# Performance work log

Measured on AMD Instinct MI355X. Metric: run time of the kernel, lower is better.

The kernel has to match this reference:

```python
import jax, jax.numpy as jnp
import numpy as np

LOG2 = float(np.log(2.0))

def _ssp(x):
    # shifted softplus: ln(0.5*(exp(x)+1)) = softplus(x) - ln 2
    return jax.nn.softplus(x) - LOG2

def setup_inputs() -> dict:
    key = jax.random.key(0)
    ks = jax.random.split(key, 8)
    B, N, D = 32, 512, 1024
    H = D // 2
    s = lambda fan_in: 1.0 / np.sqrt(fan_in)
    return {
        "representation": jax.random.normal(ks[0], (B, N, D), jnp.float32),
        "R": jax.random.normal(ks[1], (B, N, 3), jnp.float32),
        "atom_mask": jnp.ones((B, N), jnp.float32),
        "W1": jax.random.normal(ks[2], (D, H), jnp.float32) * s(D),
        "b1": jnp.zeros((H,), jnp.float32),
        "W2": jax.random.normal(ks[3], (H, 1), jnp.float32) * s(H),
        "b2": jnp.zeros((1,), jnp.float32),
        "Wc1": jax.random.normal(ks[4], (D, H), jnp.float32) * s(D),
        "bc1": jnp.zeros((H,), jnp.float32),
        "Wc2": jax.random.normal(ks[5], (H, 1), jnp.float32) * s(H),
        "bc2": jnp.zeros((1,), jnp.float32),
    }

def reference(representation, R, atom_mask, W1, b1, W2, b2, Wc1, bc1, Wc2, bc2):
    B, N, _ = representation.shape
    # Atomwise pyramidal MLP: n_in -> n_in//2 (shifted softplus) -> 1
    yi = _ssp(jnp.einsum("bnd,dh->bnh", representation, W1) + b1)
    yi = jnp.einsum("bnh,ho->bno", yi, W2) + b2            # [B,N,1]
    # masked sum pool over atoms (mean=0, stddev=1 so standardize is identity)
    y = jnp.sum(yi * atom_mask[..., None], axis=1)          # [B,1]

    # pairwise distances with safe sqrt (diag is exactly zero)
    diff = R[:, None, :, :] - R[:, :, None, :]              # [B,N,N,3]
    d2 = jnp.sum(diff * diff, axis=-1)                      # [B,N,N]
    dist = jnp.where(d2 > 0, jnp.sqrt(jnp.where(d2 > 0, d2, 1.0)), 0.0)

    eye = jnp.eye(N, dtype=dist.dtype)
    tot_mask = atom_mask[:, None, :] * atom_mask[:, :, None] * (1.0 - eye)
    keep = (tot_mask != 0).astype(dist.dtype)               # [B,N,N]
    dist = dist * keep

    # charge net: Dense(n_in, n_in//2, ssp) -> Dense(n_in//2, 1)
    q = _ssp(jnp.einsum("bnd,dh->bnh", representation, Wc1) + bc1)
    q = jnp.einsum("bnh,ho->bno", q, Wc2) + bc2             # [B,N,1]

    inv2 = (1e-5 + dist) ** -2                              # [B,N,N]
    coulomb = q[:, :, 0][:, None, :] * inv2 * q             # [B,N,N] (q_j * inv * q_i)
    coulomb = coulomb * keep
    e = jnp.sum(coulomb, axis=(1, 2))                       # [B]

    return y + e[:, None]                                   # [B,1]
```

## Files before the change

kernel.cpp:

```cpp
#include <hip/hip_runtime.h>
#include <math.h>


typedef unsigned short u16;
typedef unsigned int u32;
typedef __bf16 bf16x8 __attribute__((ext_vector_type(8)));
typedef float f32x4 __attribute__((ext_vector_type(4)));

#define GK 1024
#define NT 16

#define GLOAD_LDS16(g, l) __builtin_amdgcn_global_load_lds( \
    (const __attribute__((address_space(1))) void*)(g),     \
    (__attribute__((address_space(3))) void*)(l), 16, 0, 0)

__device__ __forceinline__ u16 f2bf(float f) {
    u32 u = __float_as_uint(f);
    return (u16)((u + 0x7FFFu + ((u >> 16) & 1u)) >> 16);
}

__device__ __forceinline__ float ssp_f(float x) {
    return __logf(0.5f * (__expf(x) + 1.0f));
}

__device__ __forceinline__ float ssp_slow(float x) {
    return fmaxf(x, 0.0f) + log1pf(expf(-fabsf(x))) - 0.6931471805599453f;
}


__global__ __launch_bounds__(256) void prep(
    const float* __restrict__ rep, const float* __restrict__ W1,
    const float* __restrict__ Wc1, u16* __restrict__ Abf,
    u16* __restrict__ Btb, float* __restrict__ out)
{
    __shared__ float tile[32][33];
    const int blk = blockIdx.x;
    const int t = threadIdx.x;
    if (blk < 8192) {
        int i = (blk * 256 + t) * 8;
        float4 x = *(const float4*)(rep + i);
        float4 y = *(const float4*)(rep + i + 4);
        union { u16 h[8]; uint4 v; } o;
        o.h[0] = f2bf(x.x); o.h[1] = f2bf(x.y); o.h[2] = f2bf(x.z); o.h[3] = f2bf(x.w);
        o.h[4] = f2bf(y.x); o.h[5] = f2bf(y.y); o.h[6] = f2bf(y.z); o.h[7] = f2bf(y.w);
        *(uint4*)(Abf + i) = o.v;
        if (blk == 0 && t < 32) out[t] = 0.0f;
    } else {
        const int bb = blk - 8192;
        const int k0 = (bb & 31) * 32;
        const int n0 = (bb >> 5) * 32;
        const float* src = (n0 < 512) ? W1 : Wc1;
        const int ns0 = (n0 < 512) ? n0 : n0 - 512;
#pragma unroll
        for (int j = 0; j < 4; j++) {
            int idx = j * 256 + t;
            int kl = idx >> 5, nl = idx & 31;
            tile[kl][nl] = src[(size_t)(k0 + kl) * 512 + ns0 + nl];
        }
        __syncthreads();
#pragma unroll
        for (int j = 0; j < 4; j++) {
            int idx = j * 256 + t;
            int nl = idx >> 5, kl = idx & 31;
            Btb[(size_t)(n0 + nl) * 1024 + k0 + kl] = f2bf(tile[kl][nl]);
        }
    }
}


__global__ __launch_bounds__(512, 2) void gemm_mfma(
    const u16* __restrict__ A,
    const u16* __restrict__ Bt,
    const float* __restrict__ b1, const float* __restrict__ W2,
    const float* __restrict__ bc1, const float* __restrict__ Wc2,
    float* __restrict__ parts)
{
    __shared__ u16 smem[2][32768];

    const int blk = blockIdx.x;
    const int swz = ((blk & 7) << 5) | (blk >> 3);
    const int bm = swz >> 2;
    const int bn = swz & 3;
    const int tid = threadIdx.x;
    const int w = tid >> 6, lane = tid & 63;
    const int wm = w & 1, wn = w >> 1;
    const int lm = lane & 15, q = lane >> 4;

    f32x4 acc[8][4];
#pragma unroll
    for (int i = 0; i < 8; i++)
#pragma unroll
        for (int j = 0; j < 4; j++)
            acc[i][j] = (f32x4){0.0f, 0.0f, 0.0f, 0.0f};

    int goff[2][2];
#pragma unroll
    for (int h = 0; h < 2; h++)
#pragma unroll
        for (int p2 = 0; p2 < 2; p2++) {
            int ci = h * 1024 + (w * 2 + p2) * 64 + lane;
            int row = ci >> 3;
            int c = (ci & 7) ^ (row & 7);
            goff[h][p2] = row * GK + c * 8;
        }

    int arow[4], brow[2], aswz[2];
#pragma unroll
    for (int mi = 0; mi < 4; mi++) arow[mi] = (wm * 128 + mi * 16 + lm) * 64;
#pragma unroll
    for (int nj = 0; nj < 2; nj++) brow[nj] = (wn * 64 + nj * 16 + lm) * 64;
#pragma unroll
    for (int kk = 0; kk < 2; kk++) aswz[kk] = ((kk * 4 + q) ^ (lm & 7)) * 8;

    const u16* Ab = A + (size_t)bm * 256 * GK;
    const u16* Bb = Bt + (size_t)bn * 256 * GK;

#define STAGE_HT(G, RG, H) do {                                               \
    GLOAD_LDS16((G) + goff[H][0], &smem[nxt][(RG) + ((H) * 1024 + (w * 2 + 0) * 64) * 8]); \
    GLOAD_LDS16((G) + goff[H][1], &smem[nxt][(RG) + ((H) * 1024 + (w * 2 + 1) * 64) * 8]); \
} while (0)

#define READ_A(MH)                                                            \
    _Pragma("unroll") for (int mi = 0; mi < 4; mi++)                          \
    _Pragma("unroll") for (int kk = 0; kk < 2; kk++)                          \
        afr[mi][kk] = *(const bf16x8*)&smem[cur][arow[mi] + (MH) * 4096 + aswz[kk]];

#define READ_B(NH)                                                            \
    _Pragma("unroll") for (int nj = 0; nj < 2; nj++)                          \
    _Pragma("unroll") for (int kk = 0; kk < 2; kk++)                          \
        bfr2[nj][kk] = *(const bf16x8*)&smem[cur][16384 + brow[nj] + (NH) * 2048 + aswz[kk]];

#define MFMA_QUAD(MH, NH)                                                     \
    _Pragma("unroll") for (int kk = 0; kk < 2; kk++)                          \
    _Pragma("unroll") for (int mi = 0; mi < 4; mi++)                          \
    _Pragma("unroll") for (int nj = 0; nj < 2; nj++)                          \
        acc[(MH) * 4 + mi][(NH) * 2 + nj] = __builtin_amdgcn_mfma_f32_16x16x32_bf16( \
            afr[mi][kk], bfr2[nj][kk], acc[(MH) * 4 + mi][(NH) * 2 + nj], 0, 0, 0);

    {
        const int nxt = 0;
#pragma unroll
        for (int h = 0; h < 2; h++) {
            STAGE_HT(Ab, 0, h);
            STAGE_HT(Bb, 16384, h);
        }
    }
    asm volatile("s_waitcnt vmcnt(0)" ::: "memory");
    __builtin_amdgcn_s_barrier();

    bf16x8 afr[4][2], bfr2[2][2];

    for (int t = 0; t < NT; ++t) {
        const int cur = t & 1, nxt = cur ^ 1;
        const bool st = (t < NT - 1);
        const u16* gA = Ab + ((t + 1) & (NT - 1)) * 64;
        const u16* gB = Bb + ((t + 1) & (NT - 1)) * 64;

        if (st) { STAGE_HT(gA, 0, 0); STAGE_HT(gB, 16384, 0); }
        READ_A(0); READ_B(0);
        __builtin_amdgcn_s_barrier();
        __builtin_amdgcn_s_setprio(1);
        MFMA_QUAD(0, 0);
        __builtin_amdgcn_s_setprio(0);
        __builtin_amdgcn_s_barrier();

        if (st) { STAGE_HT(gA, 0, 1); STAGE_HT(gB, 16384, 1); }
        READ_B(1);
        __builtin_amdgcn_s_barrier();
        __builtin_amdgcn_s_setprio(1);
        MFMA_QUAD(0, 1);
        __builtin_amdgcn_s_setprio(0);
        __builtin_amdgcn_s_barrier();

        READ_A(1);
        __builtin_amdgcn_s_barrier();
        __builtin_amdgcn_s_setprio(1);
        MFMA_QUAD(1, 1);
        __builtin_amdgcn_s_setprio(0);
        __builtin_amdgcn_s_barrier();

        READ_B(0);
        __builtin_amdgcn_s_barrier();
        __builtin_amdgcn_s_setprio(1);
        MFMA_QUAD(1, 0);
        __builtin_amdgcn_s_setprio(0);
        if (st) asm volatile("s_waitcnt vmcnt(0)" ::: "memory");
        __builtin_amdgcn_s_barrier();
    }

#undef STAGE_HT
#undef READ_A
#undef READ_B
#undef MFMA_QUAD

    __syncthreads();
    float* red = (float*)&smem[0][0];
    const bool is_q = (bn >= 2);
    const float* bb2 = is_q ? bc1 : b1;
    const float* vv = is_q ? Wc2 : W2;
    float bias[4], v[4];
#pragma unroll
    for (int nfr = 0; nfr < 4; nfr++) {
        int c = (bn & 1) * 256 + wn * 64 + nfr * 16 + lm;
        bias[nfr] = bb2[c];
        v[nfr] = vv[c];
    }
#pragma unroll
    for (int mfr = 0; mfr < 8; mfr++) {
#pragma unroll
        for (int r = 0; r < 4; r++) {
            float s = 0.0f;
#pragma unroll
            for (int nfr = 0; nfr < 4; nfr++)
                s += v[nfr] * ssp_f(acc[mfr][nfr][r] + bias[nfr]);
            s += __shfl_xor(s, 1);
            s += __shfl_xor(s, 2);
            s += __shfl_xor(s, 4);
            s += __shfl_xor(s, 8);
            if (lm == 0) red[wn * 256 + wm * 128 + mfr * 16 + q * 4 + r] = s;
        }
    }
    __syncthreads();
    if (tid < 256) {
        float val = red[0 * 256 + tid] + red[1 * 256 + tid] +
                    red[2 * 256 + tid] + red[3 * 256 + tid];
        parts[(size_t)bn * 16384 + bm * 256 + tid] = val;
    }
}


__global__ __launch_bounds__(256) void coulomb_k(
    const float* __restrict__ R, const float* __restrict__ mask,
    const float* __restrict__ parts, const float* __restrict__ b2p,
    const float* __restrict__ bc2p, float* __restrict__ out)
{
    const int N = 512;
    const int b = blockIdx.y;
    const int chunk = blockIdx.x;
    __shared__ float Rx[512], Ry[512], Rz[512], QM[512];
    __shared__ float rbuf[4];
    const int tid = threadIdx.x;
    const float bc2 = bc2p[0];
    const float b2 = b2p[0];

    for (int j = tid; j < N; j += 256) {
        int idx = b * N + j;
        float m = mask[idx];
        const float* rp = R + (size_t)idx * 3;
        Rx[j] = rp[0];
        Ry[j] = rp[1];
        Rz[j] = rp[2];
        float qv = parts[2 * 16384 + idx] + parts[3 * 16384 + idx] + bc2;
        QM[j] = qv * m;
    }
    __syncthreads();

    const int i = chunk * 64 + (tid & 63);
    const int js = (tid >> 6) * 128;
    const float xi = Rx[i], yi = Ry[i], zi = Rz[i], qmi = QM[i];
    float e = 0.0f;
    for (int j = js; j < js + 128; j++) {
        float dx = xi - Rx[j];
        float dy = yi - Ry[j];
        float dz = zi - Rz[j];
        float d2 = dx * dx + dy * dy + dz * dz;
        float t = 1e-5f + sqrtf(d2);
        float term = qmi * QM[j] / (t * t);
        e += (j == i) ? 0.0f : term;
    }
    if (tid < 64) {
        int ii = b * N + chunk * 64 + tid;
        float yv = parts[0 * 16384 + ii] + parts[1 * 16384 + ii] + b2;
        e += yv * mask[ii];
    }
    for (int off = 32; off > 0; off >>= 1) e += __shfl_down(e, off, 64);
    if ((tid & 63) == 0) rbuf[tid >> 6] = e;
    __syncthreads();
    if (tid == 0) atomicAdd(&out[b], rbuf[0] + rbuf[1] + rbuf[2] + rbuf[3]);
}


#define BM 128
#define BN 64
#define BK 16

__global__ __launch_bounds__(256) void mlp_gemm(
    const float* __restrict__ A, const float* __restrict__ W1,
    const float* __restrict__ Wc1, const float* __restrict__ b1,
    const float* __restrict__ bc1, const float* __restrict__ W2,
    const float* __restrict__ Wc2, float* __restrict__ yi_part,
    float* __restrict__ q_part)
{
    const int K = 1024;
    const int bm = blockIdx.x;
    const int bn = blockIdx.y;
    const bool is_q = (bn >= 8);
    const float* __restrict__ W = is_q ? Wc1 : W1;
    const int j0 = (bn & 7) * BN;

    __shared__ float As[BK][BM + 4];
    __shared__ float Bs[BK][BN + 4];
    __shared__ float red[BM];

    const int tid = threadIdx.x;
    const int tx = tid & 15;
    const int ty = tid >> 4;

    float acc[8][4];
#pragma unroll
    for (int r = 0; r < 8; r++)
#pragma unroll
        for (int c = 0; c < 4; c++) acc[r][c] = 0.0f;

    const int a_row = tid >> 2;
    const int a_k4 = (tid & 3) * 4;
    const float* Arow0 = A + (size_t)(bm * BM + a_row) * K;
    const float* Arow1 = Arow0 + (size_t)64 * K;
    const int w_k = tid >> 4;
    const int w_j = (tid & 15) * 4;

    for (int kt = 0; kt < K; kt += BK) {
        float4 av0 = *(const float4*)(Arow0 + kt + a_k4);
        float4 av1 = *(const float4*)(Arow1 + kt + a_k4);
        float4 wv = *(const float4*)(W + (size_t)(kt + w_k) * 512 + j0 + w_j);
        __syncthreads();
        As[a_k4 + 0][a_row] = av0.x;
        As[a_k4 + 1][a_row] = av0.y;
        As[a_k4 + 2][a_row] = av0.z;
        As[a_k4 + 3][a_row] = av0.w;
        As[a_k4 + 0][a_row + 64] = av1.x;
        As[a_k4 + 1][a_row + 64] = av1.y;
        As[a_k4 + 2][a_row + 64] = av1.z;
        As[a_k4 + 3][a_row + 64] = av1.w;
        *(float4*)&Bs[w_k][w_j] = wv;
        __syncthreads();
#pragma unroll
        for (int kk = 0; kk < BK; kk++) {
            float4 a0 = *(const float4*)&As[kk][ty * 8];
            float4 a1 = *(const float4*)&As[kk][ty * 8 + 4];
            float4 bv = *(const float4*)&Bs[kk][tx * 4];
            float ar[8] = {a0.x, a0.y, a0.z, a0.w, a1.x, a1.y, a1.z, a1.w};
            float bc[4] = {bv.x, bv.y, bv.z, bv.w};
#pragma unroll
            for (int r = 0; r < 8; r++)
#pragma unroll
                for (int c = 0; c < 4; c++)
                    acc[r][c] = fmaf(ar[r], bc[c], acc[r][c]);
        }
    }

    const float* bb = is_q ? bc1 : b1;
    const float* vv = is_q ? Wc2 : W2;
    float bias[4], v[4];
#pragma unroll
    for (int c = 0; c < 4; c++) {
        bias[c] = bb[j0 + tx * 4 + c];
        v[c] = vv[j0 + tx * 4 + c];
    }
    if (tid < BM) red[tid] = 0.0f;
    __syncthreads();
#pragma unroll
    for (int r = 0; r < 8; r++) {
        float s = 0.0f;
#pragma unroll
        for (int c = 0; c < 4; c++)
            s += v[c] * ssp_slow(acc[r][c] + bias[c]);
        atomicAdd(&red[ty * 8 + r], s);
    }
    __syncthreads();
    float* target = is_q ? q_part : yi_part;
    if (tid < BM) atomicAdd(&target[(size_t)bm * BM + tid], red[tid]);
}

__global__ __launch_bounds__(256) void coulomb_fb(
    const float* __restrict__ R, const float* __restrict__ mask,
    const float* __restrict__ yi_part, const float* __restrict__ q_part,
    const float* __restrict__ b2p, const float* __restrict__ bc2p,
    float* __restrict__ out)
{
    const int N = 512;
    const int b = blockIdx.y;
    const int chunk = blockIdx.x;
    __shared__ float Rx[512], Ry[512], Rz[512], QM[512];
    __shared__ float rbuf[4];
    const int tid = threadIdx.x;
    const float bc2 = bc2p[0];
    const float b2 = b2p[0];

    for (int j = tid; j < N; j += 256) {
        float m = mask[b * N + j];
        const float* rp = R + ((size_t)b * N + j) * 3;
        Rx[j] = rp[0];
        Ry[j] = rp[1];
        Rz[j] = rp[2];
        QM[j] = (q_part[b * N + j] + bc2) * m;
    }
    __syncthreads();

    const int i = chunk * 64 + (tid & 63);
    const int js = (tid >> 6) * 128;
    const float xi = Rx[i], yi = Ry[i], zi = Rz[i], qmi = QM[i];
    float e = 0.0f;
    for (int j = js; j < js + 128; j++) {
        float dx = xi - Rx[j];
        float dy = yi - Ry[j];
        float dz = zi - Rz[j];
        float d2 = dx * dx + dy * dy + dz * dz;
        float t = 1e-5f + sqrtf(d2);
        float term = qmi * QM[j] / (t * t);
        e += (j == i) ? 0.0f : term;
    }
    if (tid < 64) {
        int ii = chunk * 64 + tid;
        e += (yi_part[b * N + ii] + b2) * mask[b * N + ii];
    }
    for (int off = 32; off > 0; off >>= 1) e += __shfl_down(e, off, 64);
    if ((tid & 63) == 0) rbuf[tid >> 6] = e;
    __syncthreads();
    if (tid == 0) atomicAdd(&out[b], rbuf[0] + rbuf[1] + rbuf[2] + rbuf[3]);
}


extern "C" void kernel_launch(void* const* d_in, const int* in_sizes, int n_in,
                              void* d_out, int out_size, void* d_ws, size_t ws_size,
                              hipStream_t stream) {
    const float* rep  = (const float*)d_in[0];
    const float* R    = (const float*)d_in[1];
    const float* mask = (const float*)d_in[2];
    const float* W1   = (const float*)d_in[3];
    const float* b1   = (const float*)d_in[4];
    const float* W2   = (const float*)d_in[5];
    const float* b2   = (const float*)d_in[6];
    const float* Wc1  = (const float*)d_in[7];
    const float* bc1  = (const float*)d_in[8];
    const float* Wc2  = (const float*)d_in[9];
    const float* bc2  = (const float*)d_in[10];
    float* out = (float*)d_out;

    const size_t szA = 16384ull * 1024 * 2;
    const size_t szB = 1024ull * 1024 * 2;
    const size_t szP = 8ull * 16384 * 4;
    const size_t need = szA + szB + szP;

    if (ws_size >= need) {
        u16* Abf = (u16*)d_ws;
        u16* Btb = (u16*)((char*)d_ws + szA);
        float* parts = (float*)((char*)d_ws + szA + szB);

        prep<<<8192 + 1024, 256, 0, stream>>>(rep, W1, Wc1, Abf, Btb, out);
        gemm_mfma<<<256, 512, 0, stream>>>(Abf, Btb, b1, W2, bc1, Wc2, parts);
        coulomb_k<<<dim3(8, 32), 256, 0, stream>>>(R, mask, parts, b2, bc2, out);
    } else {
        float* yi_part = (float*)d_ws;
        float* q_part = yi_part + 16384;
        hipMemsetAsync(d_ws, 0, 2 * 16384 * sizeof(float), stream);
        hipMemsetAsync(d_out, 0, 32 * sizeof(float), stream);
        mlp_gemm<<<dim3(128, 16), 256, 0, stream>>>(rep, W1, Wc1, b1, bc1, W2, Wc2,
                                                    yi_part, q_part);
        coulomb_fb<<<dim3(8, 32), 256, 0, stream>>>(R, mask, yi_part, q_part, b2, bc2, out);
    }
}
```

Baseline: 169.7 us.

## Restructure GEMM main loop to one barrier per K-tile with prefetched fragments

```diff
diff --git a/kernel.cpp b/kernel.cpp
--- a/kernel.cpp
+++ b/kernel.cpp
@@ -115,77 +115,73 @@
     const u16* Ab = A + (size_t)bm * 256 * GK;
     const u16* Bb = Bt + (size_t)bn * 256 * GK;
 
-#define STAGE_HT(G, RG, H) do {                                               \
-    GLOAD_LDS16((G) + goff[H][0], &smem[nxt][(RG) + ((H) * 1024 + (w * 2 + 0) * 64) * 8]); \
-    GLOAD_LDS16((G) + goff[H][1], &smem[nxt][(RG) + ((H) * 1024 + (w * 2 + 1) * 64) * 8]); \
+#define STAGE_HT(G, RG, H, BUF) do {                                          \
+    GLOAD_LDS16((G) + goff[H][0], &smem[BUF][(RG) + ((H) * 1024 + (w * 2 + 0) * 64) * 8]); \
+    GLOAD_LDS16((G) + goff[H][1], &smem[BUF][(RG) + ((H) * 1024 + (w * 2 + 1) * 64) * 8]); \
 } while (0)
 
-#define READ_A(MH)                                                            \
+#define READ_A(BUF, MH)                                                       \
     _Pragma("unroll") for (int mi = 0; mi < 4; mi++)                          \
     _Pragma("unroll") for (int kk = 0; kk < 2; kk++)                          \
-        afr[mi][kk] = *(const bf16x8*)&smem[cur][arow[mi] + (MH) * 4096 + aswz[kk]];
-
-#define READ_B(NH)                                                            \
+        afr[mi][kk] = *(const bf16x8*)&smem[BUF][arow[mi] + (MH) * 4096 + aswz[kk]];
+
+#define READ_B(BUF, NH, DST)                                                  \
     _Pragma("unroll") for (int nj = 0; nj < 2; nj++)                          \
     _Pragma("unroll") for (int kk = 0; kk < 2; kk++)                          \
-        bfr2[nj][kk] = *(const bf16x8*)&smem[cur][16384 + brow[nj] + (NH) * 2048 + aswz[kk]];
-
-#define MFMA_QUAD(MH, NH)                                                     \
+        DST[nj][kk] = *(const bf16x8*)&smem[BUF][16384 + brow[nj] + (NH) * 2048 + aswz[kk]];
+
+#define MFMA_QUAD(MH, NH, BF)                                                 \
     _Pragma("unroll") for (int kk = 0; kk < 2; kk++)                          \
     _Pragma("unroll") for (int mi = 0; mi < 4; mi++)                          \
     _Pragma("unroll") for (int nj = 0; nj < 2; nj++)                          \
         acc[(MH) * 4 + mi][(NH) * 2 + nj] = __builtin_amdgcn_mfma_f32_16x16x32_bf16( \
-            afr[mi][kk], bfr2[nj][kk], acc[(MH) * 4 + mi][(NH) * 2 + nj], 0, 0, 0);
-
-    {
-        const int nxt = 0;
-#pragma unroll
-        for (int h = 0; h < 2; h++) {
-            STAGE_HT(Ab, 0, h);
-            STAGE_HT(Bb, 16384, h);
-        }
+            afr[mi][kk], BF[nj][kk], acc[(MH) * 4 + mi][(NH) * 2 + nj], 0, 0, 0);
+
+#pragma unroll
+    for (int h = 0; h < 2; h++) {
+        STAGE_HT(Ab, 0, h, 0);
+        STAGE_HT(Bb, 16384, h, 0);
     }
     asm volatile("s_waitcnt vmcnt(0)" ::: "memory");
     __builtin_amdgcn_s_barrier();
 
-    bf16x8 afr[4][2], bfr2[2][2];
+    bf16x8 afr[4][2], b0f[2][2], b1f[2][2];
+    READ_A(0, 0);
+    READ_B(0, 0, b0f);
 
     for (int t = 0; t < NT; ++t) {
         const int cur = t & 1, nxt = cur ^ 1;
         const bool st = (t < NT - 1);
-        const u16* gA = Ab + ((t + 1) & (NT - 1)) * 64;
-        const u16* gB = Bb + ((t + 1) & (NT - 1)) * 64;
-
-        if (st) { STAGE_HT(gA, 0, 0); STAGE_HT(gB, 16384, 0); }
-        READ_A(0); READ_B(0);
+        const u16* gA = Ab + (t + 1) * 64;
+        const u16* gB = Bb + (t + 1) * 64;
+
+        if (st) {
+            STAGE_HT(gA, 0, 0, nxt);
+            STAGE_HT(gB, 16384, 0, nxt);
+            STAGE_HT(gA, 0, 1, nxt);
+            STAGE_HT(gB, 16384, 1, nxt);
+        }
+
+        READ_B(cur, 1, b1f);
+        __builtin_amdgcn_s_setprio(1);
+        MFMA_QUAD(0, 0, b0f);
+        MFMA_QUAD(0, 1, b1f);
+        __builtin_amdgcn_s_setprio(0);
+
+        READ_A(cur, 1);
+        __builtin_amdgcn_s_setprio(1);
+        MFMA_QUAD(1, 1, b1f);
+        MFMA_QUAD(1, 0, b0f);
+        __builtin_amdgcn_s_setprio(0);
+
+        asm volatile("s_waitcnt vmcnt(0)" ::: "memory");
+        asm volatile("s_waitcnt lgkmcnt(0)" ::: "memory");
         __builtin_amdgcn_s_barrier();
-        __builtin_amdgcn_s_setprio(1);
-        MFMA_QUAD(0, 0);
-        __builtin_amdgcn_s_setprio(0);
-        __builtin_amdgcn_s_barrier();
-
-        if (st) { STAGE_HT(gA, 0, 1); STAGE_HT(gB, 16384, 1); }
-        READ_B(1);
-        __builtin_amdgcn_s_barrier();
-        __builtin_amdgcn_s_setprio(1);
-        MFMA_QUAD(0, 1);
-        __builtin_amdgcn_s_setprio(0);
-        __builtin_amdgcn_s_barrier();
-
-        READ_A(1);
-        __builtin_amdgcn_s_barrier();
-        __builtin_amdgcn_s_setprio(1);
-        MFMA_QUAD(1, 1);
-        __builtin_amdgcn_s_setprio(0);
-        __builtin_amdgcn_s_barrier();
-
-        READ_B(0);
-        __builtin_amdgcn_s_barrier();
-        __builtin_amdgcn_s_setprio(1);
-        MFMA_QUAD(1, 0);
-        __builtin_amdgcn_s_setprio(0);
-        if (st) asm volatile("s_waitcnt vmcnt(0)" ::: "memory");
-        __builtin_amdgcn_s_barrier();
+
+        if (st) {
+            READ_A(nxt, 0);
+            READ_B(nxt, 0, b0f);
+        }
     }
 
 #undef STAGE_HT
```

After: 166.1 us. 2.1% less time.
